# Kernel optimization log

Hardware: AMD Instinct MI355X
Metric: run time of the kernel (lower is better)

Reference implementation:

```python
import jax, jax.numpy as jnp
import numpy as np

C, C_H, N_HEAD = 8, 1, 8


def setup_inputs() -> dict:
    key = jax.random.key(0)
    ks = jax.random.split(key, 8)
    B, S, I, c = 1, 4096, 1024, C
    hd = C_H * N_HEAD
    m = jax.random.normal(ks[0], (B, S, I, c), dtype=jnp.float32)
    mask = jnp.ones((B, S, I), dtype=jnp.float32)
    return {
        "m": m,
        "mask": mask,
        "ln_w": jnp.ones((c,), jnp.float32),
        "ln_b": jnp.zeros((c,), jnp.float32),
        "wq": jax.random.normal(ks[1], (hd, c), jnp.float32) * 0.1,
        "wk": jax.random.normal(ks[2], (C_H, c), jnp.float32) * 0.1,
        "wv": jax.random.normal(ks[3], (C_H, c), jnp.float32) * 0.1,
        "wg": jax.random.normal(ks[4], (hd, c), jnp.float32) * 0.1,
        "bg": jnp.zeros((hd,), jnp.float32),
        "wo": jax.random.normal(ks[5], (c, hd), jnp.float32) * 0.1,
        "bo": jnp.zeros((c,), jnp.float32),
    }


def _layer_norm(x, w, b, eps=1e-5):
    mu = jnp.mean(x, axis=-1, keepdims=True)
    var = jnp.mean(jnp.square(x - mu), axis=-1, keepdims=True)
    return (x - mu) * jax.lax.rsqrt(var + eps) * w + b


def reference(m, mask, ln_w, ln_b, wq, wk, wv, wg, bg, wo, bo):
    h, c_h = N_HEAD, C_H
    # transpose so attention runs over the sequence (column) axis s
    mt = jnp.swapaxes(m, -2, -3)        # (B, i, s, c)
    mk = jnp.swapaxes(mask, -1, -2)     # (B, i, s)
    mn = _layer_norm(mt, ln_w, ln_b)    # (B, i, s, c)
    # masked mean-pooled query over s
    q = jnp.sum(mn * mk[..., None], axis=-2) / (jnp.sum(mk, axis=-1)[..., None] + 1e-5)  # (B,i,c)
    q = (q @ wq.T) * (c_h ** -0.5)                      # (B, i, h*c_h)
    q = q.reshape(*q.shape[:-1], h, c_h)                # (B, i, h, c_h)
    k = mn @ wk.T                                       # (B, i, s, c_h)
    v = mn @ wv.T                                       # (B, i, s, c_h)
    g = jax.nn.sigmoid(mn @ wg.T + bg)                  # (B, i, s, h*c_h)
    g = g.reshape(*g.shape[:-1], h, c_h)                # (B, i, s, h, c_h)
    bias = (1e9 * (mk - 1.0))[..., None, :]             # (B, i, 1, s)
    a = jnp.einsum('bihd,bisd->bihs', q, k) + bias      # (B, i, h, s)
    a = jax.nn.softmax(a, axis=-1)
    o = jnp.einsum('bihs,bisd->bihd', a, v)             # (B, i, h, c_h)
    o = o[..., None, :, :] * g                          # (B, i, s, h, c_h)
    o = o.reshape(*o.shape[:-2], h * c_h)               # (B, i, s, h*c_h)
    o = o @ wo.T + bo                                   # (B, i, s, c)
    return jnp.swapaxes(o, -2, -3)                      # (B, s, i, c)
```

## Files before the change

kernel.cpp:

```cpp
#include <hip/hip_runtime.h>

#define SS 4096
#define II 1024

#define FLAGW 254
#define QSOFF 256
#define MSOFF 8448
#define ZOFF  9472
#define NOFF  17664
#define OAOFF 25856
#define KVOFF 34048

using u16 = unsigned short;

__device__ __forceinline__ float b2f(unsigned int u) {
    union { unsigned int i; float f; } t; t.i = u << 16; return t.f;
}
__device__ __forceinline__ u16 f2b(float f) {
    union { float f; unsigned int i; } t; t.f = f;
    unsigned int x = t.i;
    return (u16)((x + 0x7fffu + ((x >> 16) & 1u)) >> 16);
}
__device__ __forceinline__ void unpack8(const uint4 p, float x[8]) {
    x[0] = b2f(p.x & 0xffffu); x[1] = b2f(p.x >> 16);
    x[2] = b2f(p.y & 0xffffu); x[3] = b2f(p.y >> 16);
    x[4] = b2f(p.z & 0xffffu); x[5] = b2f(p.z >> 16);
    x[6] = b2f(p.w & 0xffffu); x[7] = b2f(p.w >> 16);
}
__device__ __forceinline__ void load8(const void* m, size_t idx, int bf, float x[8]) {
    if (bf) {
        const uint4 p = ((const uint4*)m)[idx];
        unpack8(p, x);
    } else {
        const float4 a = ((const float4*)m)[idx * 2];
        const float4 b = ((const float4*)m)[idx * 2 + 1];
        x[0]=a.x; x[1]=a.y; x[2]=a.z; x[3]=a.w;
        x[4]=b.x; x[5]=b.y; x[6]=b.z; x[7]=b.w;
    }
}
__device__ __forceinline__ float load1(const void* p, size_t idx, int bf) {
    return bf ? b2f((unsigned int)((const u16*)p)[idx]) : ((const float*)p)[idx];
}

__global__ void wconv(const void* lnw, const void* lnb, const void* wq,
                      const void* wk,  const void* wv,  const void* wg,
                      const void* bg,  const void* wo,  const void* bo,
                      float* __restrict__ W) {
    const float probe = ((const float*)lnw)[0];
    const int bf = (fabsf(probe - 1.0f) > 1e-6f) ? 1 : 0;
    const int t = threadIdx.x;
    if (blockIdx.x == 0) {
        if (t < 8)  W[t]       = load1(lnw, t, bf);
        if (t < 8)  W[8 + t]   = load1(lnb, t, bf);
        if (t < 64) W[16 + t]  = load1(wq,  t, bf);
        if (t < 8)  W[80 + t]  = load1(wk,  t, bf);
        if (t < 8)  W[88 + t]  = load1(wv,  t, bf);
        if (t < 64) W[96 + t]  = load1(wg,  t, bf);
        if (t < 8)  W[160 + t] = load1(bg,  t, bf);
        if (t < 64) W[168 + t] = load1(wo,  t, bf);
        if (t < 8)  W[232 + t] = load1(bo,  t, bf);
        if (t == 0) W[FLAGW]   = (float)bf;
    }
    const int idx = blockIdx.x * 256 + t;
    if (idx < OAOFF - QSOFF) W[QSOFF + idx] = 0.f;
}

__global__ __launch_bounds__(256) void stage1(const void* __restrict__ m,
                                              const void* __restrict__ mask,
                                              const float* __restrict__ W,
                                              float* __restrict__ ws) {
    __shared__ float qred[4][64][8];
    __shared__ float mred[4][64];
    const int tx = threadIdx.x, ty = threadIdx.y;
    const int i  = blockIdx.x * 64 + tx;
    const int s0 = blockIdx.y * 128;
    const int bf = (int)W[FLAGW];

    float lnw[8], lnb[8], wkr[8], wvr[8];
#pragma unroll
    for (int j = 0; j < 8; j++) {
        lnw[j] = W[j]; lnb[j] = W[8 + j]; wkr[j] = W[80 + j]; wvr[j] = W[88 + j];
    }

    float2* __restrict__ kv = (float2*)(ws + KVOFF);
    float qs[8] = {0.f,0.f,0.f,0.f,0.f,0.f,0.f,0.f};
    float ms = 0.f;
#pragma unroll 4
    for (int t = 0; t < 32; t++) {
        const int s = s0 + ty + 4 * t;
        const size_t idx = (size_t)s * II + i;
        float x[8];
        load8(m, idx, bf, x);
        const float mk = load1(mask, idx, bf);
        float mu = 0.f;
#pragma unroll
        for (int j = 0; j < 8; j++) mu += x[j];
        mu *= 0.125f;
        float var = 0.f;
#pragma unroll
        for (int j = 0; j < 8; j++) { float d = x[j] - mu; var += d * d; }
        var *= 0.125f;
        const float rs = 1.0f / sqrtf(var + 1e-5f);
        float kvv = 0.f, vvv = 0.f;
#pragma unroll
        for (int j = 0; j < 8; j++) {
            const float n = (x[j] - mu) * rs * lnw[j] + lnb[j];
            kvv += wkr[j] * n;
            vvv += wvr[j] * n;
            qs[j] += n * mk;
        }
        ms += mk;
        kv[idx] = make_float2(kvv, vvv);
    }

#pragma unroll
    for (int j = 0; j < 8; j++) qred[ty][tx][j] = qs[j];
    mred[ty][tx] = ms;
    __syncthreads();
    if (ty == 0) {
#pragma unroll
        for (int j = 0; j < 8; j++) {
            const float v = qred[0][tx][j] + qred[1][tx][j] + qred[2][tx][j] + qred[3][tx][j];
            atomicAdd(&ws[QSOFF + (size_t)i * 8 + j], v);
        }
        atomicAdd(&ws[MSOFF + i], mred[0][tx] + mred[1][tx] + mred[2][tx] + mred[3][tx]);
    }
}

__global__ __launch_bounds__(256) void attnk(const void* __restrict__ mask,
                                             const float* __restrict__ W,
                                             float* __restrict__ ws) {
    __shared__ float sq[64][8];
    __shared__ float zred[4][64][8];
    __shared__ float nred[4][64][8];
    const int tx = threadIdx.x, ty = threadIdx.y;
    const int tid = ty * 64 + tx;
    const int i  = blockIdx.x * 64 + tx;
    const int s0 = blockIdx.y * 256;
    const int bf = (int)W[FLAGW];

    if (tid < 64) {
        const int i2 = blockIdx.x * 64 + tid;
        const float inv = 1.0f / (ws[MSOFF + i2] + 1e-5f);
        float qp[8];
#pragma unroll
        for (int j = 0; j < 8; j++) qp[j] = ws[QSOFF + (size_t)i2 * 8 + j] * inv;
#pragma unroll
        for (int h = 0; h < 8; h++) {
            float a = 0.f;
#pragma unroll
            for (int j = 0; j < 8; j++) a += W[16 + h * 8 + j] * qp[j];
            sq[tid][h] = a;
        }
    }
    __syncthreads();
    float qh[8];
#pragma unroll
    for (int h = 0; h < 8; h++) qh[h] = sq[tx][h];

    const float2* __restrict__ kv = (const float2*)(ws + KVOFF);
    float z[8] = {0,0,0,0,0,0,0,0}, n[8] = {0,0,0,0,0,0,0,0};
#pragma unroll 4
    for (int t = 0; t < 64; t++) {
        const int s = s0 + ty + 4 * t;
        const size_t idx = (size_t)s * II + i;
        const float2 p = kv[idx];
        const float mk = load1(mask, idx, bf);
        const float b = 1e9f * (mk - 1.0f);
#pragma unroll
        for (int h = 0; h < 8; h++) {
            const float e = __expf(qh[h] * p.x + b);
            z[h] += e;
            n[h] += e * p.y;
        }
    }
#pragma unroll
    for (int h = 0; h < 8; h++) { zred[ty][tx][h] = z[h]; nred[ty][tx][h] = n[h]; }
    __syncthreads();
    if (ty == 0) {
#pragma unroll
        for (int h = 0; h < 8; h++) {
            const float v = zred[0][tx][h] + zred[1][tx][h] + zred[2][tx][h] + zred[3][tx][h];
            atomicAdd(&ws[ZOFF + (size_t)i * 8 + h], v);
        }
    }
    if (ty == 1) {
#pragma unroll
        for (int h = 0; h < 8; h++) {
            const float v = nred[0][tx][h] + nred[1][tx][h] + nred[2][tx][h] + nred[3][tx][h];
            atomicAdd(&ws[NOFF + (size_t)i * 8 + h], v);
        }
    }
}

__global__ void oatk(float* __restrict__ ws) {
    const int idx = blockIdx.x * 256 + threadIdx.x;
    if (idx < II * 8) ws[OAOFF + idx] = ws[NOFF + idx] / ws[ZOFF + idx];
}

__global__ __launch_bounds__(256) void outk(const void* __restrict__ m,
                                            const float* __restrict__ W,
                                            const float* __restrict__ oatt,
                                            void* __restrict__ out) {
    const size_t idx = (size_t)blockIdx.x * 256 + threadIdx.x;
    const int i = (int)(idx & (II - 1));
    const int bf = (int)W[FLAGW];
    float x[8];
    load8(m, idx, bf, x);
    float mu = 0.f;
#pragma unroll
    for (int j = 0; j < 8; j++) mu += x[j];
    mu *= 0.125f;
    float var = 0.f;
#pragma unroll
    for (int j = 0; j < 8; j++) { float d = x[j] - mu; var += d * d; }
    var *= 0.125f;
    const float rs = 1.0f / sqrtf(var + 1e-5f);
    float n[8];
#pragma unroll
    for (int j = 0; j < 8; j++) n[j] = (x[j] - mu) * rs * W[j] + W[8 + j];

    float o[8];
#pragma unroll
    for (int h = 0; h < 8; h++) {
        float z = W[160 + h];
#pragma unroll
        for (int j = 0; j < 8; j++) z += W[96 + h * 8 + j] * n[j];
        const float g = 1.0f / (1.0f + __expf(-z));
        o[h] = oatt[(size_t)i * 8 + h] * g;
    }

    float y[8];
#pragma unroll
    for (int cc = 0; cc < 8; cc++) {
        float acc = W[232 + cc];
#pragma unroll
        for (int h = 0; h < 8; h++) acc += W[168 + cc * 8 + h] * o[h];
        y[cc] = acc;
    }
    if (bf) {
        u16 r[8];
#pragma unroll
        for (int cc = 0; cc < 8; cc++) r[cc] = f2b(y[cc]);
        uint4 q;
        q.x = (unsigned)r[0] | ((unsigned)r[1] << 16);
        q.y = (unsigned)r[2] | ((unsigned)r[3] << 16);
        q.z = (unsigned)r[4] | ((unsigned)r[5] << 16);
        q.w = (unsigned)r[6] | ((unsigned)r[7] << 16);
        ((uint4*)out)[idx] = q;
    } else {
        float4 a, b;
        a.x=y[0]; a.y=y[1]; a.z=y[2]; a.w=y[3];
        b.x=y[4]; b.y=y[5]; b.z=y[6]; b.w=y[7];
        ((float4*)out)[idx * 2]     = a;
        ((float4*)out)[idx * 2 + 1] = b;
    }
}

extern "C" void kernel_launch(void* const* d_in, const int* in_sizes, int n_in,
                              void* d_out, int out_size, void* d_ws, size_t ws_size,
                              hipStream_t stream) {
    float* ws = (float*)d_ws;

    wconv<<<100, 256, 0, stream>>>(d_in[2], d_in[3], d_in[4], d_in[5], d_in[6],
                                   d_in[7], d_in[8], d_in[9], d_in[10], ws);

    dim3 b1(64, 4);
    dim3 g1(II / 64, SS / 128);
    stage1<<<g1, b1, 0, stream>>>(d_in[0], d_in[1], ws, ws);

    dim3 g2(II / 64, SS / 256);
    attnk<<<g2, b1, 0, stream>>>(d_in[1], ws, ws);

    oatk<<<32, 256, 0, stream>>>(ws);

    outk<<<(SS * II) / 256, 256, 0, stream>>>(d_in[0], ws, ws + OAOFF, d_out);
}
```

Measured before the change: 318.0 us.

## Fuse stages into persistent kernel with software grid barriers

Merges the stage1, attention, normalization and output kernels into one persistent kernel of 512 blocks. The phases are separated by atomic-counter grid barriers, and the oat division is folded into the output phase. This removes the launch gaps and tail effects between kernels. In exchange it depends on all 512 blocks being co-resident to avoid deadlock, adds barrier spin cost, and changes the output phase to a strided per-thread loop.

```diff
diff --git a/kernel.cpp b/kernel.cpp
--- a/kernel.cpp
+++ b/kernel.cpp
@@ -3,6 +3,8 @@
 #define SS 4096
 #define II 1024
 
+#define CTR0  240
+#define CTR1  241
 #define FLAGW 254
 #define QSOFF 256
 #define MSOFF 8448
@@ -10,6 +12,8 @@
 #define NOFF  17664
 #define OAOFF 25856
 #define KVOFF 34048
+
+#define NBLK 512
 
 using u16 = unsigned short;
 
@@ -40,6 +44,20 @@
 }
 __device__ __forceinline__ float load1(const void* p, size_t idx, int bf) {
     return bf ? b2f((unsigned int)((const u16*)p)[idx]) : ((const float*)p)[idx];
+}
+__device__ __forceinline__ float aload(const float* p) {
+    return __hip_atomic_load(p, __ATOMIC_RELAXED, __HIP_MEMORY_SCOPE_AGENT);
+}
+__device__ __forceinline__ void gbar(unsigned* ctr) {
+    __syncthreads();
+    if (threadIdx.x == 0 && threadIdx.y == 0) {
+        __hip_atomic_fetch_add(ctr, 1u, __ATOMIC_ACQ_REL, __HIP_MEMORY_SCOPE_AGENT);
+        while (__hip_atomic_load(ctr, __ATOMIC_ACQUIRE, __HIP_MEMORY_SCOPE_AGENT)
+               < (unsigned)NBLK) {
+            __builtin_amdgcn_s_sleep(2);
+        }
+    }
+    __syncthreads();
 }
 
 __global__ void wconv(const void* lnw, const void* lnb, const void* wq,
@@ -60,200 +78,203 @@
         if (t < 64) W[168 + t] = load1(wo,  t, bf);
         if (t < 8)  W[232 + t] = load1(bo,  t, bf);
         if (t == 0) W[FLAGW]   = (float)bf;
+        if (t == 65) ((unsigned*)W)[CTR0] = 0u;
+        if (t == 66) ((unsigned*)W)[CTR1] = 0u;
     }
     const int idx = blockIdx.x * 256 + t;
     if (idx < OAOFF - QSOFF) W[QSOFF + idx] = 0.f;
 }
 
-__global__ __launch_bounds__(256) void stage1(const void* __restrict__ m,
-                                              const void* __restrict__ mask,
-                                              const float* __restrict__ W,
-                                              float* __restrict__ ws) {
-    __shared__ float qred[4][64][8];
-    __shared__ float mred[4][64];
+__global__ __launch_bounds__(256, 2) void fused(const void* __restrict__ m,
+                                                const void* __restrict__ mask,
+                                                float* ws,
+                                                void* __restrict__ out) {
+    __shared__ float smem[4608];
+    const float* W = ws;
+    const int bf = (int)W[FLAGW];
     const int tx = threadIdx.x, ty = threadIdx.y;
-    const int i  = blockIdx.x * 64 + tx;
-    const int s0 = blockIdx.y * 128;
-    const int bf = (int)W[FLAGW];
-
-    float lnw[8], lnb[8], wkr[8], wvr[8];
-#pragma unroll
-    for (int j = 0; j < 8; j++) {
-        lnw[j] = W[j]; lnb[j] = W[8 + j]; wkr[j] = W[80 + j]; wvr[j] = W[88 + j];
-    }
-
-    float2* __restrict__ kv = (float2*)(ws + KVOFF);
-    float qs[8] = {0.f,0.f,0.f,0.f,0.f,0.f,0.f,0.f};
-    float ms = 0.f;
+    const unsigned b = blockIdx.x;
+
+    {
+        const int i  = (int)(b & 15) * 64 + tx;
+        const int s0 = (int)(b >> 4) * 128;
+        float lnw[8], lnb[8], wkr[8], wvr[8];
+#pragma unroll
+        for (int j = 0; j < 8; j++) {
+            lnw[j] = W[j]; lnb[j] = W[8 + j]; wkr[j] = W[80 + j]; wvr[j] = W[88 + j];
+        }
+        float2* kv = (float2*)(ws + KVOFF);
+        float qs[8] = {0.f,0.f,0.f,0.f,0.f,0.f,0.f,0.f};
+        float msum = 0.f;
 #pragma unroll 4
-    for (int t = 0; t < 32; t++) {
-        const int s = s0 + ty + 4 * t;
-        const size_t idx = (size_t)s * II + i;
-        float x[8];
-        load8(m, idx, bf, x);
-        const float mk = load1(mask, idx, bf);
-        float mu = 0.f;
-#pragma unroll
-        for (int j = 0; j < 8; j++) mu += x[j];
-        mu *= 0.125f;
-        float var = 0.f;
-#pragma unroll
-        for (int j = 0; j < 8; j++) { float d = x[j] - mu; var += d * d; }
-        var *= 0.125f;
-        const float rs = 1.0f / sqrtf(var + 1e-5f);
-        float kvv = 0.f, vvv = 0.f;
-#pragma unroll
-        for (int j = 0; j < 8; j++) {
-            const float n = (x[j] - mu) * rs * lnw[j] + lnb[j];
-            kvv += wkr[j] * n;
-            vvv += wvr[j] * n;
-            qs[j] += n * mk;
-        }
-        ms += mk;
-        kv[idx] = make_float2(kvv, vvv);
-    }
-
-#pragma unroll
-    for (int j = 0; j < 8; j++) qred[ty][tx][j] = qs[j];
-    mred[ty][tx] = ms;
-    __syncthreads();
-    if (ty == 0) {
-#pragma unroll
-        for (int j = 0; j < 8; j++) {
-            const float v = qred[0][tx][j] + qred[1][tx][j] + qred[2][tx][j] + qred[3][tx][j];
-            atomicAdd(&ws[QSOFF + (size_t)i * 8 + j], v);
-        }
-        atomicAdd(&ws[MSOFF + i], mred[0][tx] + mred[1][tx] + mred[2][tx] + mred[3][tx]);
-    }
-}
-
-__global__ __launch_bounds__(256) void attnk(const void* __restrict__ mask,
-                                             const float* __restrict__ W,
-                                             float* __restrict__ ws) {
-    __shared__ float sq[64][8];
-    __shared__ float zred[4][64][8];
-    __shared__ float nred[4][64][8];
-    const int tx = threadIdx.x, ty = threadIdx.y;
-    const int tid = ty * 64 + tx;
-    const int i  = blockIdx.x * 64 + tx;
-    const int s0 = blockIdx.y * 256;
-    const int bf = (int)W[FLAGW];
-
-    if (tid < 64) {
-        const int i2 = blockIdx.x * 64 + tid;
-        const float inv = 1.0f / (ws[MSOFF + i2] + 1e-5f);
-        float qp[8];
-#pragma unroll
-        for (int j = 0; j < 8; j++) qp[j] = ws[QSOFF + (size_t)i2 * 8 + j] * inv;
-#pragma unroll
-        for (int h = 0; h < 8; h++) {
-            float a = 0.f;
-#pragma unroll
-            for (int j = 0; j < 8; j++) a += W[16 + h * 8 + j] * qp[j];
-            sq[tid][h] = a;
-        }
-    }
-    __syncthreads();
-    float qh[8];
-#pragma unroll
-    for (int h = 0; h < 8; h++) qh[h] = sq[tx][h];
-
-    const float2* __restrict__ kv = (const float2*)(ws + KVOFF);
-    float z[8] = {0,0,0,0,0,0,0,0}, n[8] = {0,0,0,0,0,0,0,0};
+        for (int t = 0; t < 32; t++) {
+            const int s = s0 + ty + 4 * t;
+            const size_t idx = (size_t)s * II + i;
+            float x[8];
+            load8(m, idx, bf, x);
+            const float mk = load1(mask, idx, bf);
+            float mu = 0.f;
+#pragma unroll
+            for (int j = 0; j < 8; j++) mu += x[j];
+            mu *= 0.125f;
+            float var = 0.f;
+#pragma unroll
+            for (int j = 0; j < 8; j++) { float d = x[j] - mu; var += d * d; }
+            var *= 0.125f;
+            const float rs = 1.0f / sqrtf(var + 1e-5f);
+            float kvv = 0.f, vvv = 0.f;
+#pragma unroll
+            for (int j = 0; j < 8; j++) {
+                const float nv = (x[j] - mu) * rs * lnw[j] + lnb[j];
+                kvv += wkr[j] * nv;
+                vvv += wvr[j] * nv;
+                qs[j] += nv * mk;
+            }
+            msum += mk;
+            kv[idx] = make_float2(kvv, vvv);
+        }
+        float* qred = smem;
+        float* mred = smem + 2048;
+#pragma unroll
+        for (int j = 0; j < 8; j++) qred[(ty * 64 + tx) * 8 + j] = qs[j];
+        mred[ty * 64 + tx] = msum;
+        __syncthreads();
+        if (ty == 0) {
+#pragma unroll
+            for (int j = 0; j < 8; j++) {
+                const float v = qred[tx*8+j] + qred[512+tx*8+j] + qred[1024+tx*8+j] + qred[1536+tx*8+j];
+                atomicAdd(&ws[QSOFF + (size_t)i * 8 + j], v);
+            }
+            atomicAdd(&ws[MSOFF + i], mred[tx] + mred[64+tx] + mred[128+tx] + mred[192+tx]);
+        }
+    }
+    gbar((unsigned*)ws + CTR0);
+
+    {
+        const int i0 = (int)(b & 15) * 64;
+        const int s0 = (int)(b >> 4) * 128;
+        const int tid = ty * 64 + tx;
+        float* sq   = smem;
+        float* zred = smem + 512;
+        float* nred = smem + 2560;
+        if (tid < 64) {
+            const int i2 = i0 + tid;
+            const float inv = 1.0f / (aload(&ws[MSOFF + i2]) + 1e-5f);
+            float qp[8];
+#pragma unroll
+            for (int j = 0; j < 8; j++) qp[j] = aload(&ws[QSOFF + (size_t)i2 * 8 + j]) * inv;
+#pragma unroll
+            for (int h = 0; h < 8; h++) {
+                float a = 0.f;
+#pragma unroll
+                for (int j = 0; j < 8; j++) a += W[16 + h * 8 + j] * qp[j];
+                sq[tid * 8 + h] = a;
+            }
+        }
+        __syncthreads();
+        float qh[8];
+#pragma unroll
+        for (int h = 0; h < 8; h++) qh[h] = sq[tx * 8 + h];
+
+        const float2* kv = (const float2*)(ws + KVOFF);
+        float z[8] = {0,0,0,0,0,0,0,0}, n[8] = {0,0,0,0,0,0,0,0};
 #pragma unroll 4
-    for (int t = 0; t < 64; t++) {
-        const int s = s0 + ty + 4 * t;
-        const size_t idx = (size_t)s * II + i;
-        const float2 p = kv[idx];
-        const float mk = load1(mask, idx, bf);
-        const float b = 1e9f * (mk - 1.0f);
-#pragma unroll
-        for (int h = 0; h < 8; h++) {
-            const float e = __expf(qh[h] * p.x + b);
-            z[h] += e;
-            n[h] += e * p.y;
-        }
-    }
-#pragma unroll
-    for (int h = 0; h < 8; h++) { zred[ty][tx][h] = z[h]; nred[ty][tx][h] = n[h]; }
-    __syncthreads();
-    if (ty == 0) {
-#pragma unroll
-        for (int h = 0; h < 8; h++) {
-            const float v = zred[0][tx][h] + zred[1][tx][h] + zred[2][tx][h] + zred[3][tx][h];
-            atomicAdd(&ws[ZOFF + (size_t)i * 8 + h], v);
-        }
-    }
-    if (ty == 1) {
-#pragma unroll
-        for (int h = 0; h < 8; h++) {
-            const float v = nred[0][tx][h] + nred[1][tx][h] + nred[2][tx][h] + nred[3][tx][h];
-            atomicAdd(&ws[NOFF + (size_t)i * 8 + h], v);
-        }
-    }
-}
-
-__global__ void oatk(float* __restrict__ ws) {
-    const int idx = blockIdx.x * 256 + threadIdx.x;
-    if (idx < II * 8) ws[OAOFF + idx] = ws[NOFF + idx] / ws[ZOFF + idx];
-}
-
-__global__ __launch_bounds__(256) void outk(const void* __restrict__ m,
-                                            const float* __restrict__ W,
-                                            const float* __restrict__ oatt,
-                                            void* __restrict__ out) {
-    const size_t idx = (size_t)blockIdx.x * 256 + threadIdx.x;
-    const int i = (int)(idx & (II - 1));
-    const int bf = (int)W[FLAGW];
-    float x[8];
-    load8(m, idx, bf, x);
-    float mu = 0.f;
-#pragma unroll
-    for (int j = 0; j < 8; j++) mu += x[j];
-    mu *= 0.125f;
-    float var = 0.f;
-#pragma unroll
-    for (int j = 0; j < 8; j++) { float d = x[j] - mu; var += d * d; }
-    var *= 0.125f;
-    const float rs = 1.0f / sqrtf(var + 1e-5f);
-    float n[8];
-#pragma unroll
-    for (int j = 0; j < 8; j++) n[j] = (x[j] - mu) * rs * W[j] + W[8 + j];
-
-    float o[8];
-#pragma unroll
-    for (int h = 0; h < 8; h++) {
-        float z = W[160 + h];
-#pragma unroll
-        for (int j = 0; j < 8; j++) z += W[96 + h * 8 + j] * n[j];
-        const float g = 1.0f / (1.0f + __expf(-z));
-        o[h] = oatt[(size_t)i * 8 + h] * g;
-    }
-
-    float y[8];
-#pragma unroll
-    for (int cc = 0; cc < 8; cc++) {
-        float acc = W[232 + cc];
-#pragma unroll
-        for (int h = 0; h < 8; h++) acc += W[168 + cc * 8 + h] * o[h];
-        y[cc] = acc;
-    }
-    if (bf) {
-        u16 r[8];
-#pragma unroll
-        for (int cc = 0; cc < 8; cc++) r[cc] = f2b(y[cc]);
-        uint4 q;
-        q.x = (unsigned)r[0] | ((unsigned)r[1] << 16);
-        q.y = (unsigned)r[2] | ((unsigned)r[3] << 16);
-        q.z = (unsigned)r[4] | ((unsigned)r[5] << 16);
-        q.w = (unsigned)r[6] | ((unsigned)r[7] << 16);
-        ((uint4*)out)[idx] = q;
-    } else {
-        float4 a, b;
-        a.x=y[0]; a.y=y[1]; a.z=y[2]; a.w=y[3];
-        b.x=y[4]; b.y=y[5]; b.z=y[6]; b.w=y[7];
-        ((float4*)out)[idx * 2]     = a;
-        ((float4*)out)[idx * 2 + 1] = b;
+        for (int t = 0; t < 32; t++) {
+            const int s = s0 + ty + 4 * t;
+            const size_t idx = (size_t)s * II + (i0 + tx);
+            const float2 p = kv[idx];
+            const float mk = load1(mask, idx, bf);
+            const float bb = 1e9f * (mk - 1.0f);
+#pragma unroll
+            for (int h = 0; h < 8; h++) {
+                const float e = __expf(qh[h] * p.x + bb);
+                z[h] += e;
+                n[h] += e * p.y;
+            }
+        }
+#pragma unroll
+        for (int h = 0; h < 8; h++) { zred[tid * 8 + h] = z[h]; nred[tid * 8 + h] = n[h]; }
+        __syncthreads();
+        if (ty == 0) {
+#pragma unroll
+            for (int h = 0; h < 8; h++) {
+                const float v = zred[tx*8+h] + zred[512+tx*8+h] + zred[1024+tx*8+h] + zred[1536+tx*8+h];
+                atomicAdd(&ws[ZOFF + (size_t)(i0 + tx) * 8 + h], v);
+            }
+        }
+        if (ty == 1) {
+#pragma unroll
+            for (int h = 0; h < 8; h++) {
+                const float v = nred[tx*8+h] + nred[512+tx*8+h] + nred[1024+tx*8+h] + nred[1536+tx*8+h];
+                atomicAdd(&ws[NOFF + (size_t)(i0 + tx) * 8 + h], v);
+            }
+        }
+    }
+    gbar((unsigned*)ws + CTR1);
+
+    {
+        const int tid = ty * 64 + tx;
+        const int i  = (int)(b & 3) * 256 + tid;
+        const int s0 = (int)(b >> 2) * 32;
+        float oat[8];
+#pragma unroll
+        for (int h = 0; h < 8; h++)
+            oat[h] = aload(&ws[NOFF + (size_t)i * 8 + h]) /
+                     aload(&ws[ZOFF + (size_t)i * 8 + h]);
+
+        for (int t = 0; t < 32; t++) {
+            const size_t idx = (size_t)(s0 + t) * II + i;
+            float x[8];
+            load8(m, idx, bf, x);
+            float mu = 0.f;
+#pragma unroll
+            for (int j = 0; j < 8; j++) mu += x[j];
+            mu *= 0.125f;
+            float var = 0.f;
+#pragma unroll
+            for (int j = 0; j < 8; j++) { float d = x[j] - mu; var += d * d; }
+            var *= 0.125f;
+            const float rs = 1.0f / sqrtf(var + 1e-5f);
+            float nv[8];
+#pragma unroll
+            for (int j = 0; j < 8; j++) nv[j] = (x[j] - mu) * rs * W[j] + W[8 + j];
+
+            float o[8];
+#pragma unroll
+            for (int h = 0; h < 8; h++) {
+                float zv = W[160 + h];
+#pragma unroll
+                for (int j = 0; j < 8; j++) zv += W[96 + h * 8 + j] * nv[j];
+                const float g = 1.0f / (1.0f + __expf(-zv));
+                o[h] = oat[h] * g;
+            }
+
+            float y[8];
+#pragma unroll
+            for (int cc = 0; cc < 8; cc++) {
+                float acc = W[232 + cc];
+#pragma unroll
+                for (int h = 0; h < 8; h++) acc += W[168 + cc * 8 + h] * o[h];
+                y[cc] = acc;
+            }
+            if (bf) {
+                u16 r[8];
+#pragma unroll
+                for (int cc = 0; cc < 8; cc++) r[cc] = f2b(y[cc]);
+                uint4 q;
+                q.x = (unsigned)r[0] | ((unsigned)r[1] << 16);
+                q.y = (unsigned)r[2] | ((unsigned)r[3] << 16);
+                q.z = (unsigned)r[4] | ((unsigned)r[5] << 16);
+                q.w = (unsigned)r[6] | ((unsigned)r[7] << 16);
+                ((uint4*)out)[idx] = q;
+            } else {
+                float4 a2, b2;
+                a2.x=y[0]; a2.y=y[1]; a2.z=y[2]; a2.w=y[3];
+                b2.x=y[4]; b2.y=y[5]; b2.z=y[6]; b2.w=y[7];
+                ((float4*)out)[idx * 2]     = a2;
+                ((float4*)out)[idx * 2 + 1] = b2;
+            }
+        }
     }
 }
 
@@ -265,14 +286,5 @@
     wconv<<<100, 256, 0, stream>>>(d_in[2], d_in[3], d_in[4], d_in[5], d_in[6],
                                    d_in[7], d_in[8], d_in[9], d_in[10], ws);
 
-    dim3 b1(64, 4);
-    dim3 g1(II / 64, SS / 128);
-    stage1<<<g1, b1, 0, stream>>>(d_in[0], d_in[1], ws, ws);
-
-    dim3 g2(II / 64, SS / 256);
-    attnk<<<g2, b1, 0, stream>>>(d_in[1], ws, ws);
-
-    oatk<<<32, 256, 0, stream>>>(ws);
-
-    outk<<<(SS * II) / 256, 256, 0, stream>>>(d_in[0], ws, ws + OAOFF, d_out);
-}
+    fused<<<dim3(NBLK), dim3(64, 4), 0, stream>>>(d_in[0], d_in[1], ws, d_out);
+}
```

After: 456.6 us. +43.6%, slower.
